# Kernel optimization log

Measured on AMD Instinct MI355X. Metric: run time of the kernel, lower is better.

Reference implementation:

```python
import jax, jax.numpy as jnp
import numpy as np
from jax import lax

STRIDE = (1, 1)
PADDING = ((1, 1), (1, 1))
DILATION = (1, 1)
GROUPS = 1


def setup_inputs() -> dict:
    key = jax.random.key(0)
    k1, k2, k3, k4, k5 = jax.random.split(key, 5)
    # quantized int8-ish activations/weights stored as float (as in the torch module)
    x = jax.random.randint(k1, (32, 128, 56, 56), -128, 128).astype(jnp.float32)
    weight_int = jax.random.randint(k2, (256, 128, 3, 3), -128, 128).astype(jnp.float32)
    bias_int = jax.random.randint(k3, (256,), -1024, 1024).astype(jnp.float32)
    A = jax.random.randint(k4, (256,), 1, 32768)  # per-channel requant multiplier
    N = jax.random.randint(k5, (256,), 16, 25)    # per-channel shift
    return {
        "x": x,
        "weight_int": weight_int,
        "bias_int": bias_int,
        "A": A,
        "N": N,
        "out_min": 0,
        "out_max": 255,
    }


def reference(x, weight_int, bias_int, A, N, out_min, out_max):
    # emulate torch's x.int().float() truncation casts
    xq = jnp.trunc(x)
    wq = jnp.trunc(weight_int)
    bq = jnp.trunc(bias_int)
    out = lax.conv_general_dilated(
        xq, wq,
        window_strides=STRIDE,
        padding=PADDING,
        rhs_dilation=DILATION,
        feature_group_count=GROUPS,
        dimension_numbers=("NCHW", "OIHW", "NCHW"),
    )
    out = jnp.round(out + bq[None, :, None, None])
    # out *= A ; out >>= N  (torch float rshift == divide by 2**N)
    Af = A.astype(jnp.float32)[None, :, None, None]
    Nf = N.astype(jnp.float32)[None, :, None, None]
    out = out * Af / jnp.exp2(Nf)
    if out_min >= 0:
        out = jnp.clip(jnp.round(out), float(out_min), float(out_max))
    return out
```

## Files before the change

### kernel.cpp

```cpp
#include <hip/hip_runtime.h>
#include <stdint.h>

typedef int   v4i __attribute__((ext_vector_type(4)));
typedef float v4f __attribute__((ext_vector_type(4)));

#define XT_H_STRIDE (66*128)
#define XT_N_STRIDE (58*66*128)
#define XT_BYTES    (32*58*66*128)
#define WQ_BYTES    (256*1152)

__device__ __forceinline__ void gload16(const void* g, void* l) {
  __builtin_amdgcn_global_load_lds(
      (const __attribute__((address_space(1))) void*)g,
      (__attribute__((address_space(3))) void*)l, 16, 0, 0);
}

__global__ __launch_bounds__(256) void xform_x(const float* __restrict__ x,
                                               char* __restrict__ xt) {
  __shared__ int LB[56 * 33];
  int bid = blockIdx.x;
  int n  = bid / 58;
  int hp = bid - n * 58;
  int t  = threadIdx.x;
  int srch = hp - 1;
  bool rowok = (srch >= 0) && (srch < 56);
  char* dstrow = xt + (size_t)n * XT_N_STRIDE + (size_t)hp * XT_H_STRIDE;

  if (rowok) {
    const float* rb = x + ((size_t)(n * 128) * 56 + srch) * 56;
#pragma unroll
    for (int u0 = 0; u0 < 2; ++u0) {
      int u  = t + u0 * 256;
      int wb = u & 15;
      int cb = u >> 4;
      int w0 = wb * 4, ci0 = cb * 4;
      if (w0 < 56) {
        int dw[4] = {0, 0, 0, 0};
#pragma unroll
        for (int i = 0; i < 4; ++i) {
          v4f f = *(const v4f*)(rb + (size_t)(ci0 + i) * 3136 + w0);
#pragma unroll
          for (int j = 0; j < 4; ++j)
            dw[j] |= (((int)f[j]) & 255) << (8 * i);
        }
#pragma unroll
        for (int j = 0; j < 4; ++j)
          LB[(w0 + j) * 33 + cb] = dw[j];
      }
    }
    __syncthreads();
    for (int c = t; c < 528; c += 256) {
      int wp  = c >> 3;
      int cio = c & 7;
      int srw = wp - 1;
      v4i v = {0, 0, 0, 0};
      if (srw >= 0 && srw < 56) {
#pragma unroll
        for (int k = 0; k < 4; ++k) v[k] = LB[srw * 33 + cio * 4 + k];
      }
      *(v4i*)(dstrow + c * 16) = v;
    }
  } else {
    v4i z = {0, 0, 0, 0};
    for (int c = t; c < 528; c += 256) *(v4i*)(dstrow + c * 16) = z;
  }
}

__global__ __launch_bounds__(256) void xform_w(const float* __restrict__ wsrc,
                                               const int* __restrict__ Aq,
                                               const int* __restrict__ Nq,
                                               char* __restrict__ wq2,
                                               float* __restrict__ scale) {
  int idx = blockIdx.x * 256 + threadIdx.x;
  int co = idx / 1152;
  int k  = idx - co * 1152;
  int g  = k >> 7;
  int ci = k & 127;
  int kh = g / 3;
  int kw = g - 3 * kh;
  float f = wsrc[(size_t)(co * 128 + ci) * 9 + kh * 3 + kw];
  wq2[((k >> 6) * 256 + co) * 64 + (k & 63)] = (signed char)(int)f;
  if (idx < 256) {
    scale[idx] = (float)Aq[idx] * exp2f(-(float)Nq[idx]);
  }
}

__global__ __launch_bounds__(256) void qconv_gemm(
    const char* __restrict__ xt, const char* __restrict__ wq2,
    const float* __restrict__ bias, const float* __restrict__ scale,
    const int* __restrict__ pmin, const int* __restrict__ pmax,
    float* __restrict__ out) {
  __shared__ __align__(16) char Bp[4 * 8448];
  __shared__ __align__(16) char As[2][8192];

  int bid = blockIdx.x;
  int xcd = bid & 7;
  int q   = bid >> 3;
  int mt  = q & 1;
  int nt  = xcd * 112 + (q >> 1);
  int n   = nt / 28;
  int ht  = nt - n * 28;
  int h0  = ht * 2;
  int m0  = mt * 128;

  int t  = threadIdx.x;
  int wv = t >> 6;
  int ln = t & 63;
  int quad = ln >> 4;
  int l16  = ln & 15;
  int wm = wv & 1, wn = wv >> 1;

  const char* wbase = wq2 + (size_t)m0 * 64;
  const char* xb    = xt + (size_t)n * XT_N_STRIDE + (size_t)h0 * XT_H_STRIDE;

  int a_off  = (t >> 2) * 64 + (((t & 3) ^ ((t >> 3) & 3)) * 16);
  int ldsA   = wv * 1024;

  for (int it = 0; it < 9; ++it) {
    int s = t + it * 256;
    if (s < 2112) {
      int row = s / 528;
      int rr  = s - row * 528;
      int w   = rr >> 3;
      int cq  = rr & 7;
      gload16(xb + row * XT_H_STRIDE + w * 128 + ((cq ^ (w & 7)) << 4),
              Bp + it * 4096 + wv * 1024);
    }
  }
  gload16(wbase + a_off, &As[0][ldsA]);
  gload16(wbase + 4096 + a_off, &As[0][4096 + ldsA]);
  asm volatile("s_waitcnt vmcnt(0)" ::: "memory");
  asm volatile("s_barrier" ::: "memory");

  v4i acc[4][4];
#pragma unroll
  for (int i = 0; i < 4; ++i)
#pragma unroll
    for (int j = 0; j < 4; ++j) {
      v4i z = {0, 0, 0, 0};
      acc[i][j] = z;
    }

  int ca = ((quad ^ ((l16 >> 1) & 3)) * 16);

  for (int kt = 0; kt < 18; ++kt) {
    int p  = kt & 1;
    int g  = kt >> 1;
    int kh = g / 3;
    int kw = g - 3 * kh;

    asm volatile("s_barrier" ::: "memory");
    if (kt < 17) {
      const char* wkt = wbase + ((kt + 1) << 14);
      gload16(wkt + a_off, &As[1 - p][ldsA]);
      gload16(wkt + 4096 + a_off, &As[1 - p][4096 + ldsA]);
      asm volatile("s_waitcnt vmcnt(2)" ::: "memory");
    } else {
      asm volatile("s_waitcnt vmcnt(0)" ::: "memory");
    }
    asm volatile("s_barrier" ::: "memory");

    int bswz = (((p << 2) + quad) ^ ((l16 + kw) & 7)) << 4;
    const char* bbase = Bp + (wn + kh) * XT_H_STRIDE + (l16 + kw) * 128 + bswz;

    v4i a[4], b[4];
#pragma unroll
    for (int i = 0; i < 4; ++i)
      a[i] = *(const v4i*)(&As[p][(wm * 64 + i * 16 + l16) * 64 + ca]);
#pragma unroll
    for (int j = 0; j < 4; ++j)
      b[j] = *(const v4i*)(bbase + j * 2048);
#pragma unroll
    for (int i = 0; i < 4; ++i)
#pragma unroll
      for (int j = 0; j < 4; ++j)
        acc[i][j] = __builtin_amdgcn_mfma_i32_16x16x64_i8(a[i], b[j], acc[i][j], 0, 0, 0);
  }

  float mn = (float)pmin[0];
  float mx = (float)pmax[0];
#pragma unroll
  for (int i = 0; i < 4; ++i) {
    int co_b = m0 + wm * 64 + i * 16 + quad * 4;
#pragma unroll
    for (int r = 0; r < 4; ++r) {
      int co = co_b + r;
      float bs = bias[co];
      float sc = scale[co];
#pragma unroll
      for (int j = 0; j < 4; ++j) {
        int sl = wn * 64 + j * 16 + l16;
        int w  = sl & 63;
        int dh = sl >> 6;
        if (w < 56) {
          float f = (float)acc[i][j][r] + bs;
          f = rintf(f * sc);
          f = fminf(fmaxf(f, mn), mx);
          out[(((size_t)n * 256 + co) * 56 + (h0 + dh)) * 56 + w] = f;
        }
      }
    }
  }
}

extern "C" void kernel_launch(void* const* d_in, const int* in_sizes, int n_in,
                              void* d_out, int out_size, void* d_ws, size_t ws_size,
                              hipStream_t stream) {
  const float* x  = (const float*)d_in[0];
  const float* w  = (const float*)d_in[1];
  const float* b  = (const float*)d_in[2];
  const int*   Aq = (const int*)d_in[3];
  const int*   Nq = (const int*)d_in[4];
  const int*   mn = (const int*)d_in[5];
  const int*   mx = (const int*)d_in[6];
  float* out = (float*)d_out;

  char*  xt    = (char*)d_ws;
  char*  wq2   = xt + XT_BYTES;
  float* scale = (float*)(wq2 + WQ_BYTES);

  hipLaunchKernelGGL(xform_x, dim3(32 * 58), dim3(256), 0, stream, x, xt);
  hipLaunchKernelGGL(xform_w, dim3(1152), dim3(256), 0, stream, w, Aq, Nq, wq2, scale);
  hipLaunchKernelGGL(qconv_gemm, dim3(1792), dim3(256), 0, stream,
                     xt, wq2, b, scale, mn, mx, out);
}
```

Measured before the change: 191.1 us.

## Switch GEMM to 32x32x32 MFMA with full 256-channel tile per block

```diff
diff --git a/kernel.cpp b/kernel.cpp
--- a/kernel.cpp
+++ b/kernel.cpp
@@ -1,8 +1,9 @@
 #include <hip/hip_runtime.h>
 #include <stdint.h>
 
-typedef int   v4i __attribute__((ext_vector_type(4)));
-typedef float v4f __attribute__((ext_vector_type(4)));
+typedef int   v4i  __attribute__((ext_vector_type(4)));
+typedef int   v16i __attribute__((ext_vector_type(16)));
+typedef float v4f  __attribute__((ext_vector_type(4)));
 
 #define XT_H_STRIDE (66*128)
 #define XT_N_STRIDE (58*66*128)
@@ -79,13 +80,15 @@
   int kh = g / 3;
   int kw = g - 3 * kh;
   float f = wsrc[(size_t)(co * 128 + ci) * 9 + kh * 3 + kw];
-  wq2[((k >> 6) * 256 + co) * 64 + (k & 63)] = (signed char)(int)f;
+  int kt    = g * 4 + (ci >> 5);
+  int chunk = (ci >> 4) & 1;
+  wq2[((kt * 2 + chunk) * 256 + co) * 16 + (ci & 15)] = (signed char)(int)f;
   if (idx < 256) {
     scale[idx] = (float)Aq[idx] * exp2f(-(float)Nq[idx]);
   }
 }
 
-__global__ __launch_bounds__(256) void qconv_gemm(
+__global__ __launch_bounds__(256, 2) void qconv_gemm(
     const char* __restrict__ xt, const char* __restrict__ wq2,
     const float* __restrict__ bias, const float* __restrict__ scale,
     const int* __restrict__ pmin, const int* __restrict__ pmax,
@@ -95,26 +98,20 @@
 
   int bid = blockIdx.x;
   int xcd = bid & 7;
-  int q   = bid >> 3;
-  int mt  = q & 1;
-  int nt  = xcd * 112 + (q >> 1);
+  int nt  = xcd * 112 + (bid >> 3);
   int n   = nt / 28;
   int ht  = nt - n * 28;
   int h0  = ht * 2;
-  int m0  = mt * 128;
-
-  int t  = threadIdx.x;
-  int wv = t >> 6;
-  int ln = t & 63;
-  int quad = ln >> 4;
-  int l16  = ln & 15;
-  int wm = wv & 1, wn = wv >> 1;
-
-  const char* wbase = wq2 + (size_t)m0 * 64;
+
+  int t   = threadIdx.x;
+  int wv  = t >> 6;
+  int ln  = t & 63;
+  int l31 = ln & 31;
+  int hi  = ln >> 5;
+  int wm  = wv & 1, wn = wv >> 1;
+
+  const char* wbase = wq2;
   const char* xb    = xt + (size_t)n * XT_N_STRIDE + (size_t)h0 * XT_H_STRIDE;
-
-  int a_off  = (t >> 2) * 64 + (((t & 3) ^ ((t >> 3) & 3)) * 16);
-  int ldsA   = wv * 1024;
 
   for (int it = 0; it < 9; ++it) {
     int s = t + it * 256;
@@ -127,76 +124,74 @@
               Bp + it * 4096 + wv * 1024);
     }
   }
-  gload16(wbase + a_off, &As[0][ldsA]);
-  gload16(wbase + 4096 + a_off, &As[0][4096 + ldsA]);
+  gload16(wbase + t * 16, &As[0][wv * 1024]);
+  gload16(wbase + 4096 + t * 16, &As[0][4096 + wv * 1024]);
   asm volatile("s_waitcnt vmcnt(0)" ::: "memory");
   asm volatile("s_barrier" ::: "memory");
 
-  v4i acc[4][4];
+  v16i acc[4][2];
 #pragma unroll
   for (int i = 0; i < 4; ++i)
 #pragma unroll
-    for (int j = 0; j < 4; ++j) {
-      v4i z = {0, 0, 0, 0};
+    for (int j = 0; j < 2; ++j) {
+      v16i z = {0};
       acc[i][j] = z;
     }
 
-  int ca = ((quad ^ ((l16 >> 1) & 3)) * 16);
-
-  for (int kt = 0; kt < 18; ++kt) {
-    int p  = kt & 1;
-    int g  = kt >> 1;
-    int kh = g / 3;
-    int kw = g - 3 * kh;
+  for (int kt = 0; kt < 36; ++kt) {
+    int p   = kt & 1;
+    int g   = kt >> 2;
+    int c32 = kt & 3;
+    int kh  = g / 3;
+    int kw  = g - 3 * kh;
 
     asm volatile("s_barrier" ::: "memory");
-    if (kt < 17) {
-      const char* wkt = wbase + ((kt + 1) << 14);
-      gload16(wkt + a_off, &As[1 - p][ldsA]);
-      gload16(wkt + 4096 + a_off, &As[1 - p][4096 + ldsA]);
+    if (kt < 35) {
+      const char* wkt = wbase + (kt + 1) * 8192;
+      gload16(wkt + t * 16, &As[1 - p][wv * 1024]);
+      gload16(wkt + 4096 + t * 16, &As[1 - p][4096 + wv * 1024]);
       asm volatile("s_waitcnt vmcnt(2)" ::: "memory");
     } else {
       asm volatile("s_waitcnt vmcnt(0)" ::: "memory");
     }
     asm volatile("s_barrier" ::: "memory");
 
-    int bswz = (((p << 2) + quad) ^ ((l16 + kw) & 7)) << 4;
-    const char* bbase = Bp + (wn + kh) * XT_H_STRIDE + (l16 + kw) * 128 + bswz;
-
-    v4i a[4], b[4];
-#pragma unroll
-    for (int i = 0; i < 4; ++i)
-      a[i] = *(const v4i*)(&As[p][(wm * 64 + i * 16 + l16) * 64 + ca]);
-#pragma unroll
-    for (int j = 0; j < 4; ++j)
-      b[j] = *(const v4i*)(bbase + j * 2048);
-#pragma unroll
-    for (int i = 0; i < 4; ++i)
-#pragma unroll
-      for (int j = 0; j < 4; ++j)
-        acc[i][j] = __builtin_amdgcn_mfma_i32_16x16x64_i8(a[i], b[j], acc[i][j], 0, 0, 0);
+    const char* abase = As[p] + hi * 4096 + (wm * 128 + l31) * 16;
+    int bswz = ((((c32 << 1) + hi) ^ ((l31 + kw) & 7)) << 4);
+    const char* bbase = Bp + (wn + kh) * XT_H_STRIDE + (l31 + kw) * 128 + bswz;
+
+    v4i a[4], b[2];
+#pragma unroll
+    for (int fi = 0; fi < 4; ++fi)
+      a[fi] = *(const v4i*)(abase + fi * 512);
+#pragma unroll
+    for (int fj = 0; fj < 2; ++fj)
+      b[fj] = *(const v4i*)(bbase + fj * 4096);
+#pragma unroll
+    for (int fi = 0; fi < 4; ++fi)
+#pragma unroll
+      for (int fj = 0; fj < 2; ++fj)
+        acc[fi][fj] = __builtin_amdgcn_mfma_i32_32x32x32_i8(a[fi], b[fj], acc[fi][fj], 0, 0, 0);
   }
 
   float mn = (float)pmin[0];
   float mx = (float)pmax[0];
 #pragma unroll
-  for (int i = 0; i < 4; ++i) {
-    int co_b = m0 + wm * 64 + i * 16 + quad * 4;
-#pragma unroll
-    for (int r = 0; r < 4; ++r) {
-      int co = co_b + r;
+  for (int fi = 0; fi < 4; ++fi) {
+#pragma unroll
+    for (int rg = 0; rg < 16; ++rg) {
+      int co = wm * 128 + fi * 32 + (rg & 3) + 8 * (rg >> 2) + 4 * hi;
       float bs = bias[co];
       float sc = scale[co];
-#pragma unroll
-      for (int j = 0; j < 4; ++j) {
-        int sl = wn * 64 + j * 16 + l16;
-        int w  = sl & 63;
-        int dh = sl >> 6;
+      size_t obase = ((size_t)(n * 256 + co) * 56 + (h0 + wn)) * 56;
+#pragma unroll
+      for (int fj = 0; fj < 2; ++fj) {
+        int w = fj * 32 + l31;
         if (w < 56) {
-          float f = (float)acc[i][j][r] + bs;
+          float f = (float)acc[fi][fj][rg] + bs;
           f = rintf(f * sc);
           f = fminf(fmaxf(f, mn), mx);
-          out[(((size_t)n * 256 + co) * 56 + (h0 + dh)) * 56 + w] = f;
+          out[obase + w] = f;
         }
       }
     }
@@ -221,6 +216,6 @@
 
   hipLaunchKernelGGL(xform_x, dim3(32 * 58), dim3(256), 0, stream, x, xt);
   hipLaunchKernelGGL(xform_w, dim3(1152), dim3(256), 0, stream, w, Aq, Nq, wq2, scale);
-  hipLaunchKernelGGL(qconv_gemm, dim3(1792), dim3(256), 0, stream,
+  hipLaunchKernelGGL(qconv_gemm, dim3(896), dim3(256), 0, stream,
                      xt, wq2, b, scale, mn, mx, out);
 }
```

Measured after the change: 212.4 us. +11.2%, slower.

## Load weight fragments directly into registers with prefetch, removing LDS staging and barriers

Applied to the files above, without the earlier changes.

```diff
diff --git a/kernel.cpp b/kernel.cpp
--- a/kernel.cpp
+++ b/kernel.cpp
@@ -85,13 +85,12 @@
   }
 }
 
-__global__ __launch_bounds__(256) void qconv_gemm(
+__global__ __launch_bounds__(256, 3) void qconv_gemm(
     const char* __restrict__ xt, const char* __restrict__ wq2,
     const float* __restrict__ bias, const float* __restrict__ scale,
     const int* __restrict__ pmin, const int* __restrict__ pmax,
     float* __restrict__ out) {
   __shared__ __align__(16) char Bp[4 * 8448];
-  __shared__ __align__(16) char As[2][8192];
 
   int bid = blockIdx.x;
   int xcd = bid & 7;
@@ -110,11 +109,8 @@
   int l16  = ln & 15;
   int wm = wv & 1, wn = wv >> 1;
 
-  const char* wbase = wq2 + (size_t)m0 * 64;
-  const char* xb    = xt + (size_t)n * XT_N_STRIDE + (size_t)h0 * XT_H_STRIDE;
-
-  int a_off  = (t >> 2) * 64 + (((t & 3) ^ ((t >> 3) & 3)) * 16);
-  int ldsA   = wv * 1024;
+  const char* xb = xt + (size_t)n * XT_N_STRIDE + (size_t)h0 * XT_H_STRIDE;
+  const char* abase = wq2 + (size_t)(m0 + wm * 64 + l16) * 64 + quad * 16;
 
   for (int it = 0; it < 9; ++it) {
     int s = t + it * 256;
@@ -127,10 +123,13 @@
               Bp + it * 4096 + wv * 1024);
     }
   }
-  gload16(wbase + a_off, &As[0][ldsA]);
-  gload16(wbase + 4096 + a_off, &As[0][4096 + ldsA]);
-  asm volatile("s_waitcnt vmcnt(0)" ::: "memory");
-  asm volatile("s_barrier" ::: "memory");
+
+  v4i a[4], an[4], b[4];
+#pragma unroll
+  for (int i = 0; i < 4; ++i)
+    a[i] = *(const v4i*)(abase + i * 1024);
+
+  __syncthreads();
 
   v4i acc[4][4];
 #pragma unroll
@@ -141,40 +140,35 @@
       acc[i][j] = z;
     }
 
-  int ca = ((quad ^ ((l16 >> 1) & 3)) * 16);
-
+#pragma unroll
   for (int kt = 0; kt < 18; ++kt) {
     int p  = kt & 1;
     int g  = kt >> 1;
     int kh = g / 3;
     int kw = g - 3 * kh;
 
-    asm volatile("s_barrier" ::: "memory");
     if (kt < 17) {
-      const char* wkt = wbase + ((kt + 1) << 14);
-      gload16(wkt + a_off, &As[1 - p][ldsA]);
-      gload16(wkt + 4096 + a_off, &As[1 - p][4096 + ldsA]);
-      asm volatile("s_waitcnt vmcnt(2)" ::: "memory");
-    } else {
-      asm volatile("s_waitcnt vmcnt(0)" ::: "memory");
-    }
-    asm volatile("s_barrier" ::: "memory");
+      const char* ak = abase + (size_t)(kt + 1) * 16384;
+#pragma unroll
+      for (int i = 0; i < 4; ++i)
+        an[i] = *(const v4i*)(ak + i * 1024);
+    }
 
     int bswz = (((p << 2) + quad) ^ ((l16 + kw) & 7)) << 4;
     const char* bbase = Bp + (wn + kh) * XT_H_STRIDE + (l16 + kw) * 128 + bswz;
-
-    v4i a[4], b[4];
-#pragma unroll
-    for (int i = 0; i < 4; ++i)
-      a[i] = *(const v4i*)(&As[p][(wm * 64 + i * 16 + l16) * 64 + ca]);
 #pragma unroll
     for (int j = 0; j < 4; ++j)
       b[j] = *(const v4i*)(bbase + j * 2048);
+
 #pragma unroll
     for (int i = 0; i < 4; ++i)
 #pragma unroll
       for (int j = 0; j < 4; ++j)
         acc[i][j] = __builtin_amdgcn_mfma_i32_16x16x64_i8(a[i], b[j], acc[i][j], 0, 0, 0);
+
+#pragma unroll
+    for (int i = 0; i < 4; ++i)
+      a[i] = an[i];
   }
 
   float mn = (float)pmin[0];
```

Result: slower. 197.9 us (+3.6%).
